# Optimization experiments

Hardware: AMD Instinct MI355X
Metric: run time of the kernel (lower is better)

The kernel has to match this reference:

```python
import jax, jax.numpy as jnp
import numpy as np
from jax import lax

NUM_CLASSES = 80
NUM_ANCHORS = 5
INPUT_SIZE = 1280
LAYER = 40  # INPUT_SIZE / 32
CONF_T = 0.5
IOU_T = 0.45
ANCHORS = np.array([[1.3221, 1.73145], [3.19275, 4.00944], [5.05587, 8.09892],
                    [9.47112, 4.84053], [11.2364, 10.0071]], dtype=np.float32)


def setup_inputs() -> dict:
    key = jax.random.key(0)
    x = jax.random.normal(key, (1, NUM_ANCHORS * (5 + NUM_CLASSES), LAYER, LAYER), dtype=jnp.float32)
    return {"x": x, "scaled_anchors": jnp.asarray(ANCHORS)}


def _decode(x, anchors):
    # x: (1, A*(5+C), H, W) -> boxes (N,4) in input_size scale, conf (N,), cls (N,)
    b, _, H, W = x.shape
    A = anchors.shape[0]
    stride_w = INPUT_SIZE / W
    stride_h = INPUT_SIZE / H
    pred = x.reshape(b, A, 5 + NUM_CLASSES, H, W).transpose(0, 1, 3, 4, 2)  # (b,A,H,W,5+C)
    gx, gy = jnp.meshgrid(jnp.arange(W, dtype=x.dtype), jnp.arange(H, dtype=x.dtype))
    grid = jnp.stack([gx, gy], axis=-1)  # (H,W,2)
    pxy = jax.nn.sigmoid(pred[..., 0:2]) + grid  # (b,A,H,W,2)
    pwh = jnp.exp(pred[..., 2:4]) * anchors[None, :, None, None, :]
    stride = jnp.array([stride_w, stride_h, stride_w, stride_h], dtype=x.dtype)
    pbox = jnp.concatenate([pxy, pwh], axis=-1) * stride  # (b,A,H,W,4)
    pconf = jax.nn.sigmoid(pred[..., 4])
    # sigmoid is monotonic so argmax over sigmoid(logits) == argmax over logits
    pcls = jnp.argmax(pred[..., 5:], axis=-1)
    N = A * H * W
    return pbox.reshape(N, 4), pconf.reshape(N), pcls.reshape(N)


def _nms_keep(boxes, conf, cls):
    # Greedy per-class NMS; returns fixed-shape boolean keep mask of shape (N,)
    N = boxes.shape[0]
    valid = conf > CONF_T
    cx, cy, w, h = boxes[:, 0], boxes[:, 1], boxes[:, 2], boxes[:, 3]
    x1, y1, x2, y2 = cx - w / 2, cy - h / 2, cx + w / 2, cy + h / 2
    area = jnp.maximum(x2 - x1, 0.0) * jnp.maximum(y2 - y1, 0.0)
    ix1 = jnp.maximum(x1[:, None], x1[None, :])
    iy1 = jnp.maximum(y1[:, None], y1[None, :])
    ix2 = jnp.minimum(x2[:, None], x2[None, :])
    iy2 = jnp.minimum(y2[:, None], y2[None, :])
    inter = jnp.maximum(ix2 - ix1, 0.0) * jnp.maximum(iy2 - iy1, 0.0)
    iou = inter / (area[:, None] + area[None, :] - inter + 1e-9)  # (N,N)

    score = jnp.where(valid, conf, -1.0)
    order = jnp.argsort(-score)

    def step(carry, idx):
        keep, sup = carry
        active = valid[idx] & ~sup[idx]
        keep = keep.at[idx].set(active)
        row = (iou[idx] > IOU_T) & (cls == cls[idx])
        sup = sup | (active & row)
        return (keep, sup), None

    init = (jnp.zeros(N, dtype=bool), jnp.zeros(N, dtype=bool))
    (keep, _), _ = lax.scan(step, init, order)
    return keep


def reference(x, scaled_anchors):
    boxes, conf, cls = _decode(x, scaled_anchors)
    out = jnp.concatenate([boxes, conf[:, None], cls[:, None].astype(boxes.dtype)], axis=-1)  # (N,6)
    keep = _nms_keep(boxes, conf, cls)
    # fixed-shape output: suppressed / low-confidence rows are zeroed, keep mask returned
    return out * keep[:, None].astype(out.dtype), keep
```

## Files before the change

kernel.cpp:

```cpp
#include <hip/hip_runtime.h>

#define NCLS 80
#define NA 5
#define HW 1600
#define GW 40
#define NBOX 8000
#define CONF_THR 0.5f
#define IOU_THR 0.45f
#define STRIDE_F 32.0f
#define CAP 128

#define WS_BX 0
#define WS_BY (NBOX)
#define WS_BW (2*NBOX)
#define WS_BH (3*NBOX)
#define WS_CF (4*NBOX)
#define WS_CLS (5*NBOX)

__device__ __forceinline__ float sigmoidf_(float t) {
  return 1.0f / (1.0f + expf(-t));
}

__global__ void k_decode(const float* __restrict__ x,
                         const float* __restrict__ anchors,
                         float* __restrict__ ws,
                         float* __restrict__ out) {
  int n = blockIdx.x * blockDim.x + threadIdx.x;
  if (n >= NBOX) return;
  int a = n / HW, r = n - a * HW;
  int gi = r / GW, gj = r - gi * GW;
  const float* base = x + (size_t)a * (5 + NCLS) * HW + r;

  float t0 = base[0];
  float t1 = base[HW];
  float t2 = base[2 * HW];
  float t3 = base[3 * HW];
  float t4 = base[4 * HW];
  float ax = anchors[2 * a], ay = anchors[2 * a + 1];

  float cx = (sigmoidf_(t0) + (float)gj) * STRIDE_F;
  float cy = (sigmoidf_(t1) + (float)gi) * STRIDE_F;
  float bw = (expf(t2) * ax) * STRIDE_F;
  float bh = (expf(t3) * ay) * STRIDE_F;
  float cf = sigmoidf_(t4);

  float best = base[5 * HW];
  int bi = 0;
#pragma unroll
  for (int c = 1; c < NCLS; ++c) {
    float v = base[(5 + c) * HW];
    if (v > best) { best = v; bi = c; }
  }

  ws[WS_BX + n] = cx;  ws[WS_BY + n] = cy;
  ws[WS_BW + n] = bw;  ws[WS_BH + n] = bh;
  ws[WS_CF + n] = cf;
  ((int*)(ws + WS_CLS))[n] = bi;

#pragma unroll
  for (int j = 0; j < 7; ++j) out[j * NBOX + n] = 0.0f;
}

__global__ void k_nms(const float* __restrict__ ws, float* __restrict__ out) {
  __shared__ float sconf[CAP];
  __shared__ int   slidx[CAP];
  __shared__ int   ssort[CAP];
  __shared__ float sx1[CAP], sy1[CAP], sx2[CAP], sy2[CAP], sar[CAP];

  int c = blockIdx.x, lane = threadIdx.x;
  const int*   cls = (const int*)(ws + WS_CLS);
  const float* cfp = ws + WS_CF;

  int count = 0;
  for (int base_i = 0; base_i < NBOX; base_i += 64) {
    int i = base_i + lane;
    float cfi = cfp[i];
    int ci = cls[i];
    bool pred = (cfi > CONF_THR) && (ci == c);
    unsigned long long bal = __ballot(pred);
    if (pred) {
      int pos = count + __popcll(bal & ((1ull << lane) - 1ull));
      if (pos < CAP) { sconf[pos] = cfi; slidx[pos] = i; }
    }
    count += (int)__popcll(bal);
  }
  int n = count > CAP ? CAP : count;
  __syncthreads();
  if (n <= 0) return;

  for (int p = lane; p < n; p += 64) {
    float cp = sconf[p]; int ip = slidx[p]; int rk = 0;
    for (int q = 0; q < n; ++q) {
      float cq = sconf[q];
      if (cq > cp || (cq == cp && q < p)) ++rk;
    }
    ssort[rk] = ip;
  }
  __syncthreads();

  int   gidx[2] = {-1, -1};
  float gbx[2], gby[2], gbw[2], gbh[2], gcf[2];
  float gx1[2], gy1[2], gx2[2], gy2[2], gar[2];
#pragma unroll
  for (int s = 0; s < 2; ++s) {
    int q = lane + 64 * s;
    gx1[s] = gy1[s] = gx2[s] = gy2[s] = gar[s] = 0.0f;
    if (q < n) {
      int i = ssort[q]; gidx[s] = i;
      float bx = ws[WS_BX + i], by = ws[WS_BY + i];
      float bw = ws[WS_BW + i], bh = ws[WS_BH + i];
      gbx[s] = bx; gby[s] = by; gbw[s] = bw; gbh[s] = bh;
      gcf[s] = ws[WS_CF + i];
      gx1[s] = bx - bw * 0.5f; gy1[s] = by - bh * 0.5f;
      gx2[s] = bx + bw * 0.5f; gy2[s] = by + bh * 0.5f;
      gar[s] = fmaxf(gx2[s] - gx1[s], 0.0f) * fmaxf(gy2[s] - gy1[s], 0.0f);
      sx1[q] = gx1[s]; sy1[q] = gy1[s];
      sx2[q] = gx2[s]; sy2[q] = gy2[s]; sar[q] = gar[s];
    }
  }
  __syncthreads();

  unsigned long long sup0 = 0ull, sup1 = 0ull;
  for (int p = 0; p < n; ++p) {
    unsigned long long bit = (p < 64) ? (sup0 >> p) : (sup1 >> (p - 64));
    if (bit & 1ull) continue;
    float px1 = sx1[p], py1 = sy1[p], px2 = sx2[p], py2 = sy2[p], pa = sar[p];
    bool pr0 = false, pr1 = false;
    {
      int q = lane;
      if (q > p && q < n) {
        float ix1 = fmaxf(px1, gx1[0]), iy1 = fmaxf(py1, gy1[0]);
        float ix2 = fminf(px2, gx2[0]), iy2 = fminf(py2, gy2[0]);
        float inter = fmaxf(ix2 - ix1, 0.0f) * fmaxf(iy2 - iy1, 0.0f);
        float iou = inter / (pa + gar[0] - inter + 1e-9f);
        pr0 = iou > IOU_THR;
      }
      q = lane + 64;
      if (q > p && q < n) {
        float ix1 = fmaxf(px1, gx1[1]), iy1 = fmaxf(py1, gy1[1]);
        float ix2 = fminf(px2, gx2[1]), iy2 = fminf(py2, gy2[1]);
        float inter = fmaxf(ix2 - ix1, 0.0f) * fmaxf(iy2 - iy1, 0.0f);
        float iou = inter / (pa + gar[1] - inter + 1e-9f);
        pr1 = iou > IOU_THR;
      }
    }
    sup0 |= __ballot(pr0);
    sup1 |= __ballot(pr1);
  }

#pragma unroll
  for (int s = 0; s < 2; ++s) {
    int q = lane + 64 * s;
    if (q < n) {
      unsigned long long m = s ? sup1 : sup0;
      if (!((m >> lane) & 1ull)) {
        int i = gidx[s];
        float* o = out + (size_t)i * 6;
        o[0] = gbx[s]; o[1] = gby[s]; o[2] = gbw[s]; o[3] = gbh[s];
        o[4] = gcf[s]; o[5] = (float)c;
        out[6 * NBOX + i] = 1.0f;
      }
    }
  }
}

extern "C" void kernel_launch(void* const* d_in, const int* in_sizes, int n_in,
                              void* d_out, int out_size, void* d_ws, size_t ws_size,
                              hipStream_t stream) {
  const float* x = (const float*)d_in[0];
  const float* anchors = (const float*)d_in[1];
  float* out = (float*)d_out;
  float* ws = (float*)d_ws;

  k_decode<<<(NBOX + 255) / 256, 256, 0, stream>>>(x, anchors, ws, out);
  k_nms<<<NCLS, 64, 0, stream>>>(ws, out);
}
```

Baseline: 115.3 us.

## Fuse decode and NMS into one cooperative kernel with atomic per-class buckets

Replaces the two launches with a single cooperative kernel that uses grid syncs between phases. During decode, confident boxes are appended with atomics into per-class buckets in workspace, so each class block no longer scans all 8000 boxes to compact its candidates. The block then sorts its bucket, runs wavefront-level NMS and writes the kept rows. In exchange it adds cooperative launch overhead and two grid-wide barriers. Atomic slot order is nondeterministic, so ties are now broken by box index and, when a class exceeds CAP, which boxes are kept can change.

```diff
diff --git a/kernel.cpp b/kernel.cpp
--- a/kernel.cpp
+++ b/kernel.cpp
@@ -1,4 +1,7 @@
 #include <hip/hip_runtime.h>
+#include <hip/hip_cooperative_groups.h>
+
+namespace cg = cooperative_groups;
 
 #define NCLS 80
 #define NA 5
@@ -9,124 +12,129 @@
 #define IOU_THR 0.45f
 #define STRIDE_F 32.0f
 #define CAP 128
+#define NBLK 80
+#define NTHR 256
+#define TOT (NBLK*NTHR)
 
-#define WS_BX 0
-#define WS_BY (NBOX)
-#define WS_BW (2*NBOX)
-#define WS_BH (3*NBOX)
-#define WS_CF (4*NBOX)
-#define WS_CLS (5*NBOX)
+#define WS_CNT 0
+#define WS_BKT 128
 
 __device__ __forceinline__ float sigmoidf_(float t) {
   return 1.0f / (1.0f + expf(-t));
 }
 
-__global__ void k_decode(const float* __restrict__ x,
-                         const float* __restrict__ anchors,
-                         float* __restrict__ ws,
-                         float* __restrict__ out) {
-  int n = blockIdx.x * blockDim.x + threadIdx.x;
-  if (n >= NBOX) return;
-  int a = n / HW, r = n - a * HW;
-  int gi = r / GW, gj = r - gi * GW;
-  const float* base = x + (size_t)a * (5 + NCLS) * HW + r;
+__global__ void __launch_bounds__(NTHR)
+k_fused(const float* __restrict__ x, const float* __restrict__ anchors,
+        float* __restrict__ ws, float* __restrict__ out) {
+  const int bid = blockIdx.x;
+  const int tid = threadIdx.x;
+  const int gtid = bid * NTHR + tid;
 
-  float t0 = base[0];
-  float t1 = base[HW];
-  float t2 = base[2 * HW];
-  float t3 = base[3 * HW];
-  float t4 = base[4 * HW];
-  float ax = anchors[2 * a], ay = anchors[2 * a + 1];
+  int* cnt = (int*)(ws + WS_CNT);
+  float4* bkt = (float4*)(ws + WS_BKT);
 
-  float cx = (sigmoidf_(t0) + (float)gj) * STRIDE_F;
-  float cy = (sigmoidf_(t1) + (float)gi) * STRIDE_F;
-  float bw = (expf(t2) * ax) * STRIDE_F;
-  float bh = (expf(t3) * ay) * STRIDE_F;
-  float cf = sigmoidf_(t4);
+  if (tid == 0) cnt[bid] = 0;
+  cg::this_grid().sync();
 
-  float best = base[5 * HW];
-  int bi = 0;
+  if (gtid < NBOX) {
+    const int n = gtid;
+    const int a = n / HW, r = n - a * HW;
+    const int gi = r / GW, gj = r - gi * GW;
+    const float* base = x + (size_t)a * (5 + NCLS) * HW + r;
+
+    float t0 = base[0];
+    float t1 = base[HW];
+    float t2 = base[2 * HW];
+    float t3 = base[3 * HW];
+    float t4 = base[4 * HW];
+    float ax = anchors[2 * a], ay = anchors[2 * a + 1];
+
+    float cx = (sigmoidf_(t0) + (float)gj) * STRIDE_F;
+    float cy = (sigmoidf_(t1) + (float)gi) * STRIDE_F;
+    float bw = (expf(t2) * ax) * STRIDE_F;
+    float bh = (expf(t3) * ay) * STRIDE_F;
+    float cf = sigmoidf_(t4);
+
+    float best = base[5 * HW];
+    int bi = 0;
 #pragma unroll
-  for (int c = 1; c < NCLS; ++c) {
-    float v = base[(5 + c) * HW];
-    if (v > best) { best = v; bi = c; }
+    for (int c = 1; c < NCLS; ++c) {
+      float v = base[(5 + c) * HW];
+      if (v > best) { best = v; bi = c; }
+    }
+
+    if (cf > CONF_THR) {
+      int slot = atomicAdd(cnt + bi, 1);
+      if (slot < CAP) {
+        float4 e0; e0.x = cx; e0.y = cy; e0.z = bw; e0.w = bh;
+        float4 e1; e1.x = cf; e1.y = __int_as_float(n); e1.z = 0.0f; e1.w = 0.0f;
+        bkt[(bi * CAP + slot) * 2 + 0] = e0;
+        bkt[(bi * CAP + slot) * 2 + 1] = e1;
+      }
+    }
   }
+  for (int j = gtid; j < 7 * NBOX; j += TOT) out[j] = 0.0f;
 
-  ws[WS_BX + n] = cx;  ws[WS_BY + n] = cy;
-  ws[WS_BW + n] = bw;  ws[WS_BH + n] = bh;
-  ws[WS_CF + n] = cf;
-  ((int*)(ws + WS_CLS))[n] = bi;
+  cg::this_grid().sync();
 
-#pragma unroll
-  for (int j = 0; j < 7; ++j) out[j * NBOX + n] = 0.0f;
-}
+  __shared__ float4 ent[CAP * 2];
+  __shared__ int ssort[CAP];
+  __shared__ float sx1[CAP], sy1[CAP], sx2[CAP], sy2[CAP], sar[CAP];
+  __shared__ float4 sbox[CAP];
+  __shared__ float scf[CAP];
+  __shared__ int sidx[CAP];
+  __shared__ unsigned long long smask[2];
 
-__global__ void k_nms(const float* __restrict__ ws, float* __restrict__ out) {
-  __shared__ float sconf[CAP];
-  __shared__ int   slidx[CAP];
-  __shared__ int   ssort[CAP];
-  __shared__ float sx1[CAP], sy1[CAP], sx2[CAP], sy2[CAP], sar[CAP];
+  const int c = bid;
+  int n = cnt[c];
+  if (n > CAP) n = CAP;
 
-  int c = blockIdx.x, lane = threadIdx.x;
-  const int*   cls = (const int*)(ws + WS_CLS);
-  const float* cfp = ws + WS_CF;
+  for (int k = tid; k < 2 * n; k += NTHR) ent[k] = bkt[c * CAP * 2 + k];
+  __syncthreads();
 
-  int count = 0;
-  for (int base_i = 0; base_i < NBOX; base_i += 64) {
-    int i = base_i + lane;
-    float cfi = cfp[i];
-    int ci = cls[i];
-    bool pred = (cfi > CONF_THR) && (ci == c);
-    unsigned long long bal = __ballot(pred);
-    if (pred) {
-      int pos = count + __popcll(bal & ((1ull << lane) - 1ull));
-      if (pos < CAP) { sconf[pos] = cfi; slidx[pos] = i; }
+  if (tid < n) {
+    float cp = ent[2 * tid + 1].x;
+    int ip = __float_as_int(ent[2 * tid + 1].y);
+    int rk = 0;
+    for (int q = 0; q < n; ++q) {
+      float cq = ent[2 * q + 1].x;
+      int iq = __float_as_int(ent[2 * q + 1].y);
+      if (cq > cp || (cq == cp && iq < ip)) ++rk;
     }
-    count += (int)__popcll(bal);
-  }
-  int n = count > CAP ? CAP : count;
-  __syncthreads();
-  if (n <= 0) return;
-
-  for (int p = lane; p < n; p += 64) {
-    float cp = sconf[p]; int ip = slidx[p]; int rk = 0;
-    for (int q = 0; q < n; ++q) {
-      float cq = sconf[q];
-      if (cq > cp || (cq == cp && q < p)) ++rk;
-    }
-    ssort[rk] = ip;
+    ssort[rk] = tid;
   }
   __syncthreads();
 
-  int   gidx[2] = {-1, -1};
-  float gbx[2], gby[2], gbw[2], gbh[2], gcf[2];
-  float gx1[2], gy1[2], gx2[2], gy2[2], gar[2];
-#pragma unroll
-  for (int s = 0; s < 2; ++s) {
-    int q = lane + 64 * s;
-    gx1[s] = gy1[s] = gx2[s] = gy2[s] = gar[s] = 0.0f;
-    if (q < n) {
-      int i = ssort[q]; gidx[s] = i;
-      float bx = ws[WS_BX + i], by = ws[WS_BY + i];
-      float bw = ws[WS_BW + i], bh = ws[WS_BH + i];
-      gbx[s] = bx; gby[s] = by; gbw[s] = bw; gbh[s] = bh;
-      gcf[s] = ws[WS_CF + i];
-      gx1[s] = bx - bw * 0.5f; gy1[s] = by - bh * 0.5f;
-      gx2[s] = bx + bw * 0.5f; gy2[s] = by + bh * 0.5f;
-      gar[s] = fmaxf(gx2[s] - gx1[s], 0.0f) * fmaxf(gy2[s] - gy1[s], 0.0f);
-      sx1[q] = gx1[s]; sy1[q] = gy1[s];
-      sx2[q] = gx2[s]; sy2[q] = gy2[s]; sar[q] = gar[s];
-    }
+  if (tid < n) {
+    int b = ssort[tid];
+    float4 box = ent[2 * b + 0];
+    float4 meta = ent[2 * b + 1];
+    float x1 = box.x - box.z * 0.5f, y1 = box.y - box.w * 0.5f;
+    float x2 = box.x + box.z * 0.5f, y2 = box.y + box.w * 0.5f;
+    sx1[tid] = x1; sy1[tid] = y1; sx2[tid] = x2; sy2[tid] = y2;
+    sar[tid] = fmaxf(x2 - x1, 0.0f) * fmaxf(y2 - y1, 0.0f);
+    sbox[tid] = box; scf[tid] = meta.x; sidx[tid] = __float_as_int(meta.y);
   }
   __syncthreads();
 
-  unsigned long long sup0 = 0ull, sup1 = 0ull;
-  for (int p = 0; p < n; ++p) {
-    unsigned long long bit = (p < 64) ? (sup0 >> p) : (sup1 >> (p - 64));
-    if (bit & 1ull) continue;
-    float px1 = sx1[p], py1 = sy1[p], px2 = sx2[p], py2 = sy2[p], pa = sar[p];
-    bool pr0 = false, pr1 = false;
-    {
+  if (tid < 64) {
+    const int lane = tid;
+    float gx1[2], gy1[2], gx2[2], gy2[2], gar[2];
+#pragma unroll
+    for (int s = 0; s < 2; ++s) {
+      int q = lane + 64 * s;
+      gx1[s] = gy1[s] = gx2[s] = gy2[s] = gar[s] = 0.0f;
+      if (q < n) {
+        gx1[s] = sx1[q]; gy1[s] = sy1[q];
+        gx2[s] = sx2[q]; gy2[s] = sy2[q]; gar[s] = sar[q];
+      }
+    }
+    unsigned long long sup0 = 0ull, sup1 = 0ull;
+    for (int p = 0; p < n; ++p) {
+      unsigned long long bit = (p < 64) ? (sup0 >> p) : (sup1 >> (p - 64));
+      if (bit & 1ull) continue;
+      float px1 = sx1[p], py1 = sy1[p], px2 = sx2[p], py2 = sy2[p], pa = sar[p];
+      bool pr0 = false, pr1 = false;
       int q = lane;
       if (q > p && q < n) {
         float ix1 = fmaxf(px1, gx1[0]), iy1 = fmaxf(py1, gy1[0]);
@@ -143,23 +151,21 @@
         float iou = inter / (pa + gar[1] - inter + 1e-9f);
         pr1 = iou > IOU_THR;
       }
+      sup0 |= __ballot(pr0);
+      sup1 |= __ballot(pr1);
     }
-    sup0 |= __ballot(pr0);
-    sup1 |= __ballot(pr1);
+    if (lane == 0) { smask[0] = sup0; smask[1] = sup1; }
   }
+  __syncthreads();
 
-#pragma unroll
-  for (int s = 0; s < 2; ++s) {
-    int q = lane + 64 * s;
-    if (q < n) {
-      unsigned long long m = s ? sup1 : sup0;
-      if (!((m >> lane) & 1ull)) {
-        int i = gidx[s];
-        float* o = out + (size_t)i * 6;
-        o[0] = gbx[s]; o[1] = gby[s]; o[2] = gbw[s]; o[3] = gbh[s];
-        o[4] = gcf[s]; o[5] = (float)c;
-        out[6 * NBOX + i] = 1.0f;
-      }
+  if (tid < n) {
+    if (!((smask[tid >> 6] >> (tid & 63)) & 1ull)) {
+      int i = sidx[tid];
+      float4 b = sbox[tid];
+      float* o = out + (size_t)i * 6;
+      o[0] = b.x; o[1] = b.y; o[2] = b.z; o[3] = b.w;
+      o[4] = scf[tid]; o[5] = (float)c;
+      out[6 * NBOX + i] = 1.0f;
     }
   }
 }
@@ -172,6 +178,7 @@
   float* out = (float*)d_out;
   float* ws = (float*)d_ws;
 
-  k_decode<<<(NBOX + 255) / 256, 256, 0, stream>>>(x, anchors, ws, out);
-  k_nms<<<NCLS, 64, 0, stream>>>(ws, out);
+  void* args[] = {(void*)&x, (void*)&anchors, (void*)&ws, (void*)&out};
+  hipLaunchCooperativeKernel((const void*)k_fused, dim3(NBLK), dim3(NTHR),
+                             args, 0, stream);
 }
```

Result: no change. 116.9 us (+1.4%).
